# Kernel tuning notes

Measured on AMD Instinct MI355X. Metric: run time of the kernel, lower is better.

## Reference

```python
import jax, jax.numpy as jnp
import numpy as np

NEG_INF = -1e30
LRELU_SLOPE = 0.2

B, E, IN_DIM, OUT_DIM = 64, 512, 1024, 256


def setup_inputs() -> dict:
    key = jax.random.key(0)
    ks = jax.random.split(key, 6)
    input_state = jax.random.normal(ks[0], (B, E, IN_DIM), dtype=jnp.float32)
    adj = jnp.ones((B, E, E), dtype=jnp.float32)  # only used via ones_like in the original
    node_mask = jax.random.randint(ks[1], (B, E, 1), 0, 2, dtype=jnp.int32)
    W_w = jax.random.normal(ks[2], (OUT_DIM, IN_DIM), dtype=jnp.float32) * (1.0 / np.sqrt(IN_DIM))
    W_b = jax.random.normal(ks[3], (OUT_DIM,), dtype=jnp.float32) * 0.02
    a_w = jax.random.normal(ks[4], (1, 2 * OUT_DIM), dtype=jnp.float32) * (1.0 / np.sqrt(2 * OUT_DIM))
    a_b = jax.random.normal(ks[5], (1,), dtype=jnp.float32) * 0.02
    return {"input_state": input_state, "adj": adj, "node_mask": node_mask,
            "W_w": W_w, "W_b": W_b, "a_w": a_w, "a_b": a_b}


def reference(input_state, adj, node_mask, W_w, W_b, a_w, a_b):
    # h = W(input_state); dropout is identity in eval mode (gnn_drop=0)
    h = jnp.einsum('bei,oi->beo', input_state, W_w) + W_b  # b,E,d
    d = h.shape[-1]
    # a([h_i ; h_j]) decomposes exactly: a_w[:, :d] @ h_i + a_w[:, d:] @ h_j + a_b
    a1, a2 = a_w[:, :d], a_w[:, d:]
    s1 = jnp.einsum('beo,xo->bex', h, a1)  # b,E,1 -> score contribution of source node i
    s2 = jnp.einsum('beo,xo->bex', h, a2)  # b,E,1 -> contribution of target node j
    scores = s1 + jnp.swapaxes(s2, 1, 2) + a_b  # b,E,E, scores[n,i,j] = a([h_i;h_j])
    scores = jnp.where(scores >= 0, scores, LRELU_SLOPE * scores)  # LeakyReLU(0.2)
    # fully-connected adjacency gated by node mask: mask_i * mask_j
    m = node_mask.astype(scores.dtype)  # b,E,1
    pair_mask = m * jnp.swapaxes(m, 1, 2)  # b,E,E
    scores = jnp.where(pair_mask > 0, scores, NEG_INF)
    coefs = jax.nn.softmax(scores, axis=-1)  # b,E,E
    h = h * m  # zero out masked nodes before aggregation
    return jnp.einsum('bij,bjo->bio', coefs, h)
```

## Files before the change

kernel.cpp:

```cpp
#include <hip/hip_runtime.h>
#include <hip/hip_fp16.h>
#include <math.h>

#define NEG_INF_F (-1e30f)
#define LRELU 0.2f

constexpr int Bb = 64, Ee = 512, IND = 1024, OUTD = 256;
constexpr int Mrows = Bb * Ee;

typedef __attribute__((ext_vector_type(8))) _Float16 half8;
typedef __attribute__((ext_vector_type(4))) _Float16 half4;
typedef __attribute__((ext_vector_type(4))) float floatx4;

#define AS1 __attribute__((address_space(1)))
#define AS3 __attribute__((address_space(3)))

__global__ __launch_bounds__(256) void wconv_kernel(
    const float* __restrict__ W, _Float16* __restrict__ Whf)
{
    const int i = (blockIdx.x * 256 + threadIdx.x) * 4;
    const float4 w = *reinterpret_cast<const float4*>(&W[i]);
    half4 hh;
    hh[0] = (_Float16)w.x; hh[1] = (_Float16)w.y;
    hh[2] = (_Float16)w.z; hh[3] = (_Float16)w.w;
    *reinterpret_cast<half4*>(&Whf[i]) = hh;
}

__global__ __launch_bounds__(512, 4) void gemm_h_f16(
    const float* __restrict__ X, const _Float16* __restrict__ Whf,
    const float* __restrict__ Wb, const float* __restrict__ aw,
    const int* __restrict__ mask,
    _Float16* __restrict__ HmTh, float* __restrict__ s1, float* __restrict__ s2)
{
    __shared__ char lds_raw[73728];
    float*    Af  = (float*)lds_raw;
    _Float16* Bf  = (_Float16*)(lds_raw + 24576);
    _Float16* Th   = (_Float16*)lds_raw;
    float*    s1p  = (float*)(lds_raw + 32768);
    float*    s2p  = (float*)(lds_raw + 33792);
    float*    mkfs = (float*)(lds_raw + 34816);

    const int t  = threadIdx.x;
    const int w  = t >> 6, l = t & 63, ln = l & 15, lg = l >> 4;
    const int wr = w >> 2, wc = w & 3;
    const int m0 = blockIdx.x * 64;

    const int arl = l >> 3;
    const int agl = (l & 7) ^ arl;
    const int brl = l >> 2;
    const int bgl = (l & 3) ^ ((l >> 3) & 3);

    floatx4 acc[2][4];
    #pragma unroll
    for (int i = 0; i < 2; ++i)
        #pragma unroll
        for (int j = 0; j < 4; ++j)
            acc[i][j] = (floatx4)0.f;

    auto stageA = [&](int kc, int aoff) {
        const size_t src = (size_t)(m0 + w * 8 + arl) * IND + kc * 32 + agl * 4;
        __builtin_amdgcn_global_load_lds(
            (const AS1 unsigned int*)(X + src),
            (AS3 unsigned int*)(Af + aoff + w * 8 * 32), 16, 0, 0);
    };
    auto stageB = [&](int kc, int boff) {
        #pragma unroll
        for (int i = 0; i < 2; ++i) {
            const int nbase = w * 32 + i * 16;
            const size_t src = (size_t)(nbase + brl) * IND + kc * 32 + bgl * 8;
            __builtin_amdgcn_global_load_lds(
                (const AS1 unsigned int*)(Whf + src),
                (AS3 unsigned int*)(Bf + boff + nbase * 32), 16, 0, 0);
        }
    };

    int aO0 = 0, aO1 = 2048, aO2 = 4096;
    int bO0 = 0, bO1 = 8192, bO2 = 16384;

    stageA(0, aO0); stageB(0, bO0);
    stageA(1, aO1); stageB(1, bO1);
    asm volatile("s_waitcnt vmcnt(3) lgkmcnt(0)" ::: "memory");
    __builtin_amdgcn_sched_barrier(0);
    __builtin_amdgcn_s_barrier();
    __builtin_amdgcn_sched_barrier(0);

    for (int ts = 0; ts < 32; ++ts) {
        if (ts < 30) { stageA(ts + 2, aO2); stageB(ts + 2, bO2); }
        __builtin_amdgcn_sched_barrier(0);

        half8 bfrag[4];
        #pragma unroll
        for (int nr = 0; nr < 4; ++nr) {
            const int n = wc * 64 + nr * 16 + ln;
            const int phys = lg ^ ((n >> 1) & 3);
            bfrag[nr] = *reinterpret_cast<const half8*>(Bf + bO0 + n * 32 + phys * 8);
        }
        half8 afrag[2];
        #pragma unroll
        for (int mr = 0; mr < 2; ++mr) {
            const int r = wr * 32 + mr * 16 + ln;
            const int g0 = (lg * 2) ^ (r & 7);
            const int g1 = (lg * 2 + 1) ^ (r & 7);
            const floatx4 a0 = *reinterpret_cast<const floatx4*>(Af + aO0 + r * 32 + g0 * 4);
            const floatx4 a1 = *reinterpret_cast<const floatx4*>(Af + aO0 + r * 32 + g1 * 4);
            half8 h;
            h[0] = (_Float16)a0[0]; h[1] = (_Float16)a0[1];
            h[2] = (_Float16)a0[2]; h[3] = (_Float16)a0[3];
            h[4] = (_Float16)a1[0]; h[5] = (_Float16)a1[1];
            h[6] = (_Float16)a1[2]; h[7] = (_Float16)a1[3];
            afrag[mr] = h;
        }

        __builtin_amdgcn_s_setprio(1);
        #pragma unroll
        for (int mr = 0; mr < 2; ++mr)
            #pragma unroll
            for (int nr = 0; nr < 4; ++nr)
                acc[mr][nr] = __builtin_amdgcn_mfma_f32_16x16x32_f16(
                    afrag[mr], bfrag[nr], acc[mr][nr], 0, 0, 0);
        __builtin_amdgcn_s_setprio(0);

        if (ts < 30) asm volatile("s_waitcnt vmcnt(3) lgkmcnt(0)" ::: "memory");
        else         asm volatile("s_waitcnt vmcnt(0) lgkmcnt(0)" ::: "memory");
        __builtin_amdgcn_sched_barrier(0);
        __builtin_amdgcn_s_barrier();
        __builtin_amdgcn_sched_barrier(0);

        int tmp = aO0; aO0 = aO1; aO1 = aO2; aO2 = tmp;
        tmp = bO0; bO0 = bO1; bO1 = bO2; bO2 = tmp;
    }

    if (t < 64) mkfs[t] = (float)mask[m0 + t];

    float bias[4], a1c[4], a2c[4];
    #pragma unroll
    for (int nr = 0; nr < 4; ++nr) {
        const int n = wc * 64 + nr * 16 + ln;
        bias[nr] = Wb[n];
        a1c[nr]  = aw[n];
        a2c[nr]  = aw[OUTD + n];
    }
    float sv1[2][4], sv2[2][4];
    #pragma unroll
    for (int i = 0; i < 2; ++i)
        #pragma unroll
        for (int r = 0; r < 4; ++r) { sv1[i][r] = 0.f; sv2[i][r] = 0.f; }

    #pragma unroll
    for (int mr = 0; mr < 2; ++mr)
        #pragma unroll
        for (int nr = 0; nr < 4; ++nr) {
            const int o = wc * 64 + nr * 16 + ln;
            half4 hh;
            #pragma unroll
            for (int rr = 0; rr < 4; ++rr) {
                const float hb = acc[mr][nr][rr] + bias[nr];
                sv1[mr][rr] += hb * a1c[nr];
                sv2[mr][rr] += hb * a2c[nr];
                hh[rr] = (_Float16)hb;
            }
            const int e = wr * 32 + mr * 16 + lg * 4;
            *reinterpret_cast<half4*>(Th + o * 64 + (e ^ ((o & 7) << 3))) = hh;
        }

    #pragma unroll
    for (int mr = 0; mr < 2; ++mr)
        #pragma unroll
        for (int rr = 0; rr < 4; ++rr) {
            float v1 = sv1[mr][rr], v2 = sv2[mr][rr];
            #pragma unroll
            for (int off = 1; off < 16; off <<= 1) {
                v1 += __shfl_xor(v1, off, 64);
                v2 += __shfl_xor(v2, off, 64);
            }
            if (ln == 0) {
                const int el = mr * 16 + lg * 4 + rr;
                s1p[w * 32 + el] = v1;
                s2p[w * 32 + el] = v2;
            }
        }
    __syncthreads();

    if (t < 64) {
        const int wrr = t >> 5, el = t & 31;
        const int b0 = (wrr * 4) * 32 + el;
        s1[m0 + t] = s1p[b0] + s1p[b0 + 32] + s1p[b0 + 64] + s1p[b0 + 96];
        s2[m0 + t] = s2p[b0] + s2p[b0 + 32] + s2p[b0 + 64] + s2p[b0 + 96];
    }

    const int bIdx = m0 >> 9;
    const int e0   = m0 & 511;
    const int e4   = (t & 15) * 4;
    const float q0 = mkfs[e4 + 0], q1 = mkfs[e4 + 1];
    const float q2 = mkfs[e4 + 2], q3 = mkfs[e4 + 3];
    #pragma unroll
    for (int it = 0; it < 8; ++it) {
        const int o = it * 32 + (t >> 4);
        half4 vh = *reinterpret_cast<const half4*>(Th + o * 64 + (e4 ^ ((o & 7) << 3)));
        if (!(q0 > 0.f)) vh[0] = (_Float16)0.f;
        if (!(q1 > 0.f)) vh[1] = (_Float16)0.f;
        if (!(q2 > 0.f)) vh[2] = (_Float16)0.f;
        if (!(q3 > 0.f)) vh[3] = (_Float16)0.f;
        const size_t goff = ((size_t)(bIdx * OUTD + o) << 9) + e0 + e4;
        *reinterpret_cast<half4*>(&HmTh[goff]) = vh;
    }
}

__global__ __launch_bounds__(256, 2) void attn_mfma(
    const _Float16* __restrict__ HmTh,
    const float* __restrict__ s1, const float* __restrict__ s2,
    const int* __restrict__ mask, const float* __restrict__ ab_ptr,
    float* __restrict__ Out)
{
    __shared__ float s2v[Ee];
    __shared__ float mkv[Ee];
    __shared__ float rowc[64];
    __shared__ float rmax[64];
    __shared__ int   rvv[64];
    __shared__ _Float16 Pl[2][64][32];
    __shared__ float Zp[64][4];
    __shared__ float zr[64];
    __shared__ float wmax[4];

    const int bid = blockIdx.x;
    const int b  = bid & 63;
    const int i0 = (bid >> 6) * 64;
    const int t  = threadIdx.x;
    const int w  = t >> 6, l = t & 63, ln = l & 15, lg = l >> 4;
    const float ab = ab_ptr[0];

    float lmax = -INFINITY;
    #pragma unroll
    for (int q = 0; q < 2; ++q) {
        const int j = t + q * 256;
        const float sv = s2[b * Ee + j];
        const float mv = (float)mask[b * Ee + j];
        s2v[j] = sv; mkv[j] = mv;
        if (mv > 0.f) lmax = fmaxf(lmax, sv);
    }
    #pragma unroll
    for (int off = 32; off; off >>= 1) lmax = fmaxf(lmax, __shfl_xor(lmax, off, 64));
    if (l == 0) wmax[w] = lmax;
    __syncthreads();
    const float s2max = fmaxf(fmaxf(wmax[0], wmax[1]), fmaxf(wmax[2], wmax[3]));
    const int anyvalid = (s2max > -1e37f) ? 1 : 0;
    if (t < 64) {
        const float c = s1[b * Ee + i0 + t] + ab;
        rowc[t] = c;
        const int mi = mask[b * Ee + i0 + t];
        rvv[t] = (mi != 0) & anyvalid;
        const float rm = c + s2max;
        rmax[t] = (rm >= 0.f) ? rm : LRELU * rm;
    }
    __syncthreads();

    const int pi = t >> 2;
    const int pj = (t & 3) * 8;
    const float prc = rowc[pi];
    const float prm = rmax[pi];
    const int   prv = rvv[pi];
    float zacc = 0.f;

    const size_t obase = (size_t)b * OUTD * Ee;
    const int o0 = w * 64;

    floatx4 acc[4][4];
    #pragma unroll
    for (int i = 0; i < 4; ++i)
        #pragma unroll
        for (int j = 0; j < 4; ++j)
            acc[i][j] = (floatx4)0.f;

    for (int ks = 0; ks < 16; ++ks) {
        const int k0  = ks * 32;
        const int buf = ks & 1;

        half8 ph;
        #pragma unroll
        for (int kk = 0; kk < 8; ++kk) {
            const int j = k0 + pj + kk;
            float pv;
            if (prv) {
                float sc = prc + s2v[j];
                sc = (sc >= 0.f) ? sc : LRELU * sc;
                pv = (mkv[j] > 0.f) ? __expf(sc - prm) : 0.f;
            } else {
                pv = 1.f;
            }
            const _Float16 hq = (_Float16)pv;
            ph[kk] = hq;
            zacc += (float)hq;
        }
        *reinterpret_cast<half8*>(&Pl[buf][pi][pj]) = ph;

        half8 bh[4];
        #pragma unroll
        for (int ot = 0; ot < 4; ++ot) {
            const size_t ro = obase + (size_t)(o0 + ot * 16 + ln) * Ee + k0 + lg * 8;
            bh[ot] = *reinterpret_cast<const half8*>(&HmTh[ro]);
        }
        __syncthreads();

        half8 af[4];
        #pragma unroll
        for (int mr = 0; mr < 4; ++mr)
            af[mr] = *reinterpret_cast<const half8*>(&Pl[buf][mr * 16 + ln][lg * 8]);
        #pragma unroll
        for (int mr = 0; mr < 4; ++mr)
            #pragma unroll
            for (int ot = 0; ot < 4; ++ot)
                acc[mr][ot] = __builtin_amdgcn_mfma_f32_16x16x32_f16(
                    af[mr], bh[ot], acc[mr][ot], 0, 0, 0);
    }

    Zp[pi][t & 3] = zacc;
    __syncthreads();
    if (t < 64) {
        const float z = Zp[t][0] + Zp[t][1] + Zp[t][2] + Zp[t][3];
        zr[t] = 1.f / z;
    }
    __syncthreads();

    float* __restrict__ Ob = Out + ((size_t)b * Ee + i0) * OUTD;
    #pragma unroll
    for (int mr = 0; mr < 4; ++mr)
        #pragma unroll
        for (int rr = 0; rr < 4; ++rr) {
            const int i = mr * 16 + lg * 4 + rr;
            const float rzi = zr[i];
            #pragma unroll
            for (int ot = 0; ot < 4; ++ot)
                Ob[(size_t)i * OUTD + o0 + ot * 16 + ln] = acc[mr][ot][rr] * rzi;
        }
}

extern "C" void kernel_launch(void* const* d_in, const int* in_sizes, int n_in,
                              void* d_out, int out_size, void* d_ws, size_t ws_size,
                              hipStream_t stream) {
    const float* X    = (const float*)d_in[0];
    const int*   mask = (const int*)d_in[2];
    const float* Ww   = (const float*)d_in[3];
    const float* Wb   = (const float*)d_in[4];
    const float* aw   = (const float*)d_in[5];
    const float* ab   = (const float*)d_in[6];
    float* out = (float*)d_out;

    _Float16* HmTh = (_Float16*)d_ws;
    float* s1 = (float*)(HmTh + (size_t)Bb * OUTD * Ee);
    float* s2 = s1 + Mrows;
    _Float16* Whf = (_Float16*)(s2 + Mrows);

    wconv_kernel<<<OUTD * IND / (256 * 4), 256, 0, stream>>>(Ww, Whf);
    gemm_h_f16<<<Mrows / 64, 512, 0, stream>>>(X, Whf, Wb, aw, mask, HmTh, s1, s2);
    attn_mfma<<<Bb * (Ee / 64), 256, 0, stream>>>(HmTh, s1, s2, mask, ab, out);
}
```

Before: 72.83 us.

## Preload whole fp16 A tile into LDS once and double-buffer only B

Replaces the per-k-step fp32 A staging (triple buffered via global_load_lds, converted to fp16 inside the loop) with an upfront load of the block's entire 64x1024 X tile. It is converted to fp16 and stored swizzled in 128KB of LDS. The B (weight) pipeline drops to double buffering with a full vmcnt(0) wait each step. This removes repeated fp32->fp16 conversions and halves A LDS traffic, but needs 160KB LDS so only one block fits per CU. The prologue load is also serialized before any compute, so there is less overlap and lower occupancy.

```diff
diff --git a/kernel.cpp b/kernel.cpp
--- a/kernel.cpp
+++ b/kernel.cpp
@@ -26,43 +26,28 @@
     *reinterpret_cast<half4*>(&Whf[i]) = hh;
 }
 
-__global__ __launch_bounds__(512, 4) void gemm_h_f16(
+__global__ __launch_bounds__(512, 1) void gemm_h_f16(
     const float* __restrict__ X, const _Float16* __restrict__ Whf,
     const float* __restrict__ Wb, const float* __restrict__ aw,
     const int* __restrict__ mask,
     _Float16* __restrict__ HmTh, float* __restrict__ s1, float* __restrict__ s2)
 {
-    __shared__ char lds_raw[73728];
-    float*    Af  = (float*)lds_raw;
-    _Float16* Bf  = (_Float16*)(lds_raw + 24576);
-    _Float16* Th   = (_Float16*)lds_raw;
-    float*    s1p  = (float*)(lds_raw + 32768);
-    float*    s2p  = (float*)(lds_raw + 33792);
-    float*    mkfs = (float*)(lds_raw + 34816);
+    __shared__ char lds_raw[163840];
+    _Float16* Ah = (_Float16*)lds_raw;
+    _Float16* Bf = (_Float16*)(lds_raw + 131072);
+    _Float16* Th   = (_Float16*)(lds_raw + 131072);
+    float*    s1p  = (float*)lds_raw;
+    float*    s2p  = (float*)(lds_raw + 1024);
+    float*    mkfs = (float*)(lds_raw + 2048);
 
     const int t  = threadIdx.x;
     const int w  = t >> 6, l = t & 63, ln = l & 15, lg = l >> 4;
     const int wr = w >> 2, wc = w & 3;
     const int m0 = blockIdx.x * 64;
 
-    const int arl = l >> 3;
-    const int agl = (l & 7) ^ arl;
     const int brl = l >> 2;
     const int bgl = (l & 3) ^ ((l >> 3) & 3);
 
-    floatx4 acc[2][4];
-    #pragma unroll
-    for (int i = 0; i < 2; ++i)
-        #pragma unroll
-        for (int j = 0; j < 4; ++j)
-            acc[i][j] = (floatx4)0.f;
-
-    auto stageA = [&](int kc, int aoff) {
-        const size_t src = (size_t)(m0 + w * 8 + arl) * IND + kc * 32 + agl * 4;
-        __builtin_amdgcn_global_load_lds(
-            (const AS1 unsigned int*)(X + src),
-            (AS3 unsigned int*)(Af + aoff + w * 8 * 32), 16, 0, 0);
-    };
     auto stageB = [&](int kc, int boff) {
         #pragma unroll
         for (int i = 0; i < 2; ++i) {
@@ -74,18 +59,38 @@
         }
     };
 
-    int aO0 = 0, aO1 = 2048, aO2 = 4096;
-    int bO0 = 0, bO1 = 8192, bO2 = 16384;
-
-    stageA(0, aO0); stageB(0, bO0);
-    stageA(1, aO1); stageB(1, bO1);
-    asm volatile("s_waitcnt vmcnt(3) lgkmcnt(0)" ::: "memory");
-    __builtin_amdgcn_sched_barrier(0);
-    __builtin_amdgcn_s_barrier();
-    __builtin_amdgcn_sched_barrier(0);
+    stageB(0, 0);
+
+    {
+        const int prow = w * 8 + (l >> 3);
+        const int ps   = l & 7;
+        const float* __restrict__ xsrc = X + (size_t)(m0 + prow) * IND + ps * 8;
+        _Float16* __restrict__ adst = Ah + prow * 1024;
+        #pragma unroll 4
+        for (int ii = 0; ii < 16; ++ii) {
+            const float4 u0 = *reinterpret_cast<const float4*>(xsrc + ii * 64);
+            const float4 u1 = *reinterpret_cast<const float4*>(xsrc + ii * 64 + 4);
+            half8 h;
+            h[0] = (_Float16)u0.x; h[1] = (_Float16)u0.y;
+            h[2] = (_Float16)u0.z; h[3] = (_Float16)u0.w;
+            h[4] = (_Float16)u1.x; h[5] = (_Float16)u1.y;
+            h[6] = (_Float16)u1.z; h[7] = (_Float16)u1.w;
+            const int phys = ii * 8 + (ps ^ (prow & 7));
+            *reinterpret_cast<half8*>(adst + phys * 8) = h;
+        }
+    }
+    __syncthreads();
+
+    floatx4 acc[2][4];
+    #pragma unroll
+    for (int i = 0; i < 2; ++i)
+        #pragma unroll
+        for (int j = 0; j < 4; ++j)
+            acc[i][j] = (floatx4)0.f;
 
     for (int ts = 0; ts < 32; ++ts) {
-        if (ts < 30) { stageA(ts + 2, aO2); stageB(ts + 2, bO2); }
+        const int cur = (ts & 1) * 8192;
+        if (ts < 31) stageB(ts + 1, 8192 - cur);
         __builtin_amdgcn_sched_barrier(0);
 
         half8 bfrag[4];
@@ -93,22 +98,14 @@
         for (int nr = 0; nr < 4; ++nr) {
             const int n = wc * 64 + nr * 16 + ln;
             const int phys = lg ^ ((n >> 1) & 3);
-            bfrag[nr] = *reinterpret_cast<const half8*>(Bf + bO0 + n * 32 + phys * 8);
+            bfrag[nr] = *reinterpret_cast<const half8*>(Bf + cur + n * 32 + phys * 8);
         }
         half8 afrag[2];
         #pragma unroll
         for (int mr = 0; mr < 2; ++mr) {
             const int r = wr * 32 + mr * 16 + ln;
-            const int g0 = (lg * 2) ^ (r & 7);
-            const int g1 = (lg * 2 + 1) ^ (r & 7);
-            const floatx4 a0 = *reinterpret_cast<const floatx4*>(Af + aO0 + r * 32 + g0 * 4);
-            const floatx4 a1 = *reinterpret_cast<const floatx4*>(Af + aO0 + r * 32 + g1 * 4);
-            half8 h;
-            h[0] = (_Float16)a0[0]; h[1] = (_Float16)a0[1];
-            h[2] = (_Float16)a0[2]; h[3] = (_Float16)a0[3];
-            h[4] = (_Float16)a1[0]; h[5] = (_Float16)a1[1];
-            h[6] = (_Float16)a1[2]; h[7] = (_Float16)a1[3];
-            afrag[mr] = h;
+            const int gphys = (ts >> 1) * 8 + (((ts & 1) * 4 + lg) ^ (r & 7));
+            afrag[mr] = *reinterpret_cast<const half8*>(Ah + r * 1024 + gphys * 8);
         }
 
         __builtin_amdgcn_s_setprio(1);
@@ -120,14 +117,10 @@
                     afrag[mr], bfrag[nr], acc[mr][nr], 0, 0, 0);
         __builtin_amdgcn_s_setprio(0);
 
-        if (ts < 30) asm volatile("s_waitcnt vmcnt(3) lgkmcnt(0)" ::: "memory");
-        else         asm volatile("s_waitcnt vmcnt(0) lgkmcnt(0)" ::: "memory");
+        asm volatile("s_waitcnt vmcnt(0) lgkmcnt(0)" ::: "memory");
         __builtin_amdgcn_sched_barrier(0);
         __builtin_amdgcn_s_barrier();
         __builtin_amdgcn_sched_barrier(0);
-
-        int tmp = aO0; aO0 = aO1; aO1 = aO2; aO2 = tmp;
-        tmp = bO0; bO0 = bO1; bO1 = bO2; bO2 = tmp;
     }
 
     if (t < 64) mkfs[t] = (float)mask[m0 + t];
```

Measured after the change: 91.76 us. 1.26x slower.
